# Kernel optimization log

Hardware: AMD Instinct MI355X
Metric: run time of the kernel (lower is better)

## Reference

```python
import jax, jax.numpy as jnp
import numpy as np

B, TE, TD, HE, HD = 4, 512, 256, 128, 256

def setup_inputs() -> dict:
    key = jax.random.key(0)
    k1, k2, k3, k4, k5 = jax.random.split(key, 5)
    return {
        "encoder_out_seq": jax.random.normal(k1, (B, TE, HE), dtype=jnp.float32),
        "decoder_out_seq": jax.random.normal(k2, (B, TD, HD), dtype=jnp.float32),
        "W_a": jax.random.normal(k3, (HE, HE), dtype=jnp.float32) * 0.05,
        "U_a": jax.random.normal(k4, (HD, HE), dtype=jnp.float32) * 0.05,
        "V_a": jax.random.normal(k5, (HE, 1), dtype=jnp.float32) * 0.05,
    }

def reference(encoder_out_seq, decoder_out_seq, W_a, U_a, V_a):
    # Bahdanau additive attention, fully parallel over decoder steps
    # (the original K.rnn scan has no true recurrence: each step is independent).
    Ws = jnp.einsum('bse,ef->bsf', encoder_out_seq, W_a)   # [B,Te,He]
    Uh = jnp.einsum('btd,df->btf', decoder_out_seq, U_a)   # [B,Td,He]
    # [B,Td,Te,He] additive score features
    feat = jnp.tanh(Ws[:, None, :, :] + Uh[:, :, None, :])
    e = jnp.einsum('btsf,f->bts', feat, V_a[:, 0])         # [B,Td,Te]
    e = jax.nn.softmax(e, axis=-1)                         # attention weights
    c = jnp.einsum('bts,bse->bte', e, encoder_out_seq)     # [B,Td,He] contexts
    return (c, e)
```

## Files before the change

kernel.cpp:

```cpp
#include <hip/hip_runtime.h>

#define Bn  4
#define TEn 512
#define TDn 256
#define HEn 128
#define HDn 256

#define KSCALE 2.8853900817779268f

#if __has_builtin(__builtin_amdgcn_exp2f)
#define EXP2(x) __builtin_amdgcn_exp2f(x)
#else
#define EXP2(x) __expf(0.6931471805599453f * (x))
#endif

__device__ __forceinline__ float sigEP(float E, float P) {
    return __builtin_amdgcn_rcpf(fmaf(E, P, 1.0f));
}

__global__ __launch_bounds__(512) void ws_gemm_kernel(
    const float* __restrict__ enc, const float* __restrict__ W,
    float* __restrict__ Ws)
{
    __shared__ __align__(16) float enc_lds[4 * HEn];
    const int tid = threadIdx.x;
    const int c   = tid & (HEn - 1);
    const int rl  = tid >> 7;
    const int r0  = blockIdx.x * 4;
    enc_lds[tid] = enc[r0 * HEn + tid];
    __syncthreads();
    const float* wc = W + c;
    const float* er = enc_lds + rl * HEn;
    float acc = 0.f;
    #pragma unroll 4
    for (int k = 0; k < HEn; k += 8) {
        float4 e0 = *(const float4*)(er + k);
        float4 e1 = *(const float4*)(er + k + 4);
        acc = fmaf(e0.x, wc[(k + 0) * HEn], acc);
        acc = fmaf(e0.y, wc[(k + 1) * HEn], acc);
        acc = fmaf(e0.z, wc[(k + 2) * HEn], acc);
        acc = fmaf(e0.w, wc[(k + 3) * HEn], acc);
        acc = fmaf(e1.x, wc[(k + 4) * HEn], acc);
        acc = fmaf(e1.y, wc[(k + 5) * HEn], acc);
        acc = fmaf(e1.z, wc[(k + 6) * HEn], acc);
        acc = fmaf(e1.w, wc[(k + 7) * HEn], acc);
    }
    Ws[(r0 + rl) * HEn + c] = acc * KSCALE;
}

__global__ __launch_bounds__(1024, 4) void attn_kernel(
    const float* __restrict__ enc, const float* __restrict__ dec,
    const float* __restrict__ U, const float* __restrict__ V,
    const float* __restrict__ Ws, float* __restrict__ c_out,
    float* __restrict__ e_out)
{
    const int b    = blockIdx.x >> 6;
    const int t0   = (blockIdx.x & 63) * 4;
    const int bt0  = b * TDn + t0;
    const int tid  = threadIdx.x;
    const int lane = tid & 63;
    const int wave = tid >> 6;

    __shared__ __align__(16) float dec_lds[4 * HDn];
    __shared__ __align__(16) float uh[4][HEn];
    __shared__ __align__(16) float sc[4][TEn];
    __shared__ __align__(16) float part[32][512];
    __shared__ float redm[4][8];
    __shared__ float reds[4][8];

    dec_lds[tid] = dec[bt0 * HDn + tid];
    __syncthreads();

    {
        const int f = tid & 127;
        const int p = tid >> 7;
        const float* u = U + (p * 32) * HEn + f;
        float a0 = 0.f, a1 = 0.f, a2 = 0.f, a3 = 0.f;
        #pragma unroll 8
        for (int k = 0; k < 32; ++k) {
            const float uk = u[k * HEn];
            const int kk = p * 32 + k;
            a0 = fmaf(dec_lds[kk],            uk, a0);
            a1 = fmaf(dec_lds[HDn + kk],      uk, a1);
            a2 = fmaf(dec_lds[2 * HDn + kk],  uk, a2);
            a3 = fmaf(dec_lds[3 * HDn + kk],  uk, a3);
        }
        part[p][f]       = a0;
        part[p][128 + f] = a1;
        part[p][256 + f] = a2;
        part[p][384 + f] = a3;
    }
    __syncthreads();
    if (tid < 512) {
        const int r = tid >> 7, f = tid & 127;
        float s0 = 0.f, s1 = 0.f;
        #pragma unroll
        for (int p = 0; p < 8; p += 2) {
            s0 += part[p][r * 128 + f];
            s1 += part[p + 1][r * 128 + f];
        }
        uh[r][f] = EXP2((s0 + s1) * KSCALE);
    }
    __syncthreads();

    {
        const int s_sub = lane & 7;
        const int f0    = (lane >> 3) * 16;
        float4 vn[4], uu[4][4];
        float sv = 0.f;
        #pragma unroll
        for (int j = 0; j < 4; ++j) {
            float4 v = *(const float4*)(V + f0 + 4 * j);
            sv += v.x + v.y + v.z + v.w;
            vn[j] = make_float4(-2.f * v.x, -2.f * v.y, -2.f * v.z, -2.f * v.w);
            #pragma unroll
            for (int r = 0; r < 4; ++r)
                uu[r][j] = *(const float4*)(&uh[r][f0 + 4 * j]);
        }
        const float* wsb = Ws + (b * TEn + wave * 32) * HEn;
        #pragma unroll
        for (int ci = 0; ci < 4; ++ci) {
            const float* wp = wsb + (ci * 8 + s_sub) * HEn + f0;
            float x0 = sv, x1 = sv, x2 = sv, x3 = sv;
            #pragma unroll
            for (int j = 0; j < 4; ++j) {
                float4 w = ((const float4*)wp)[j];
                const float Ex = EXP2(w.x);
                const float Ey = EXP2(w.y);
                const float Ez = EXP2(w.z);
                const float Ew = EXP2(w.w);
                x0 = fmaf(vn[j].x, sigEP(Ex, uu[0][j].x), x0);
                x1 = fmaf(vn[j].x, sigEP(Ex, uu[1][j].x), x1);
                x2 = fmaf(vn[j].x, sigEP(Ex, uu[2][j].x), x2);
                x3 = fmaf(vn[j].x, sigEP(Ex, uu[3][j].x), x3);
                x0 = fmaf(vn[j].y, sigEP(Ey, uu[0][j].y), x0);
                x1 = fmaf(vn[j].y, sigEP(Ey, uu[1][j].y), x1);
                x2 = fmaf(vn[j].y, sigEP(Ey, uu[2][j].y), x2);
                x3 = fmaf(vn[j].y, sigEP(Ey, uu[3][j].y), x3);
                x0 = fmaf(vn[j].z, sigEP(Ez, uu[0][j].z), x0);
                x1 = fmaf(vn[j].z, sigEP(Ez, uu[1][j].z), x1);
                x2 = fmaf(vn[j].z, sigEP(Ez, uu[2][j].z), x2);
                x3 = fmaf(vn[j].z, sigEP(Ez, uu[3][j].z), x3);
                x0 = fmaf(vn[j].w, sigEP(Ew, uu[0][j].w), x0);
                x1 = fmaf(vn[j].w, sigEP(Ew, uu[1][j].w), x1);
                x2 = fmaf(vn[j].w, sigEP(Ew, uu[2][j].w), x2);
                x3 = fmaf(vn[j].w, sigEP(Ew, uu[3][j].w), x3);
            }
            x0 += __shfl_xor(x0, 8, 64);  x1 += __shfl_xor(x1, 8, 64);
            x2 += __shfl_xor(x2, 8, 64);  x3 += __shfl_xor(x3, 8, 64);
            x0 += __shfl_xor(x0, 16, 64); x1 += __shfl_xor(x1, 16, 64);
            x2 += __shfl_xor(x2, 16, 64); x3 += __shfl_xor(x3, 16, 64);
            x0 += __shfl_xor(x0, 32, 64); x1 += __shfl_xor(x1, 32, 64);
            x2 += __shfl_xor(x2, 32, 64); x3 += __shfl_xor(x3, 32, 64);
            if (lane < 8) {
                const int s = wave * 32 + ci * 8 + lane;
                sc[0][s] = x0; sc[1][s] = x1; sc[2][s] = x2; sc[3][s] = x3;
            }
        }
    }
    __syncthreads();

    {
        const int s  = tid & 511;
        const int r0 = (tid >> 9) * 2;
        const int w8 = wave & 7;
        const float v0 = sc[r0][s];
        const float v1 = sc[r0 + 1][s];
        float m0 = v0, m1 = v1;
        #pragma unroll
        for (int off = 32; off; off >>= 1) {
            m0 = fmaxf(m0, __shfl_xor(m0, off, 64));
            m1 = fmaxf(m1, __shfl_xor(m1, off, 64));
        }
        if (lane == 0) { redm[r0][w8] = m0; redm[r0 + 1][w8] = m1; }
        __syncthreads();
        float bm0 = redm[r0][0], bm1 = redm[r0 + 1][0];
        #pragma unroll
        for (int w = 1; w < 8; ++w) {
            bm0 = fmaxf(bm0, redm[r0][w]);
            bm1 = fmaxf(bm1, redm[r0 + 1][w]);
        }
        const float ex0 = __expf(v0 - bm0);
        const float ex1 = __expf(v1 - bm1);
        float s0 = ex0, s1 = ex1;
        #pragma unroll
        for (int off = 32; off; off >>= 1) {
            s0 += __shfl_xor(s0, off, 64);
            s1 += __shfl_xor(s1, off, 64);
        }
        if (lane == 0) { reds[r0][w8] = s0; reds[r0 + 1][w8] = s1; }
        __syncthreads();
        float bs0 = reds[r0][0], bs1 = reds[r0 + 1][0];
        #pragma unroll
        for (int w = 1; w < 8; ++w) { bs0 += reds[r0][w]; bs1 += reds[r0 + 1][w]; }
        const float e0 = ex0 * __builtin_amdgcn_rcpf(bs0);
        const float e1 = ex1 * __builtin_amdgcn_rcpf(bs1);
        e_out[(bt0 + r0) * TEn + s]     = e0;
        e_out[(bt0 + r0 + 1) * TEn + s] = e1;
        sc[r0][s]     = e0;
        sc[r0 + 1][s] = e1;
    }
    __syncthreads();

    {
        const int hl = tid & 31;
        const int sp = tid >> 5;
        const float* eb = enc + (b * TEn + sp * 16) * HEn + hl * 4;
        float4 a0 = {0,0,0,0}, a1 = {0,0,0,0}, a2 = {0,0,0,0}, a3 = {0,0,0,0};
        #pragma unroll 4
        for (int i = 0; i < 16; ++i) {
            const int s = sp * 16 + i;
            const float4 ev = *(const float4*)(eb + i * HEn);
            const float w0 = sc[0][s], w1 = sc[1][s];
            const float w2 = sc[2][s], w3 = sc[3][s];
            a0.x = fmaf(w0, ev.x, a0.x); a1.x = fmaf(w1, ev.x, a1.x);
            a2.x = fmaf(w2, ev.x, a2.x); a3.x = fmaf(w3, ev.x, a3.x);
            a0.y = fmaf(w0, ev.y, a0.y); a1.y = fmaf(w1, ev.y, a1.y);
            a2.y = fmaf(w2, ev.y, a2.y); a3.y = fmaf(w3, ev.y, a3.y);
            a0.z = fmaf(w0, ev.z, a0.z); a1.z = fmaf(w1, ev.z, a1.z);
            a2.z = fmaf(w2, ev.z, a2.z); a3.z = fmaf(w3, ev.z, a3.z);
            a0.w = fmaf(w0, ev.w, a0.w); a1.w = fmaf(w1, ev.w, a1.w);
            a2.w = fmaf(w2, ev.w, a2.w); a3.w = fmaf(w3, ev.w, a3.w);
        }
        *(float4*)&part[sp][0   + hl * 4] = a0;
        *(float4*)&part[sp][128 + hl * 4] = a1;
        *(float4*)&part[sp][256 + hl * 4] = a2;
        *(float4*)&part[sp][384 + hl * 4] = a3;
    }
    __syncthreads();
    if (tid < 512) {
        const int r = tid >> 7, h = tid & 127;
        float s0 = 0.f, s1 = 0.f;
        #pragma unroll
        for (int p = 0; p < 32; p += 2) {
            s0 += part[p][r * 128 + h];
            s1 += part[p + 1][r * 128 + h];
        }
        c_out[(bt0 + r) * HEn + h] = s0 + s1;
    }
}

extern "C" void kernel_launch(void* const* d_in, const int* in_sizes, int n_in,
                              void* d_out, int out_size, void* d_ws, size_t ws_size,
                              hipStream_t stream) {
    const float* enc = (const float*)d_in[0];
    const float* dec = (const float*)d_in[1];
    const float* W   = (const float*)d_in[2];
    const float* U   = (const float*)d_in[3];
    const float* V   = (const float*)d_in[4];
    float* out   = (float*)d_out;
    float* c_out = out;
    float* e_out = out + Bn * TDn * HEn;
    float* Ws    = (float*)d_ws;

    ws_gemm_kernel<<<(Bn * TEn) / 4, 512, 0, stream>>>(enc, W, Ws);
    attn_kernel<<<(Bn * TDn) / 4, 1024, 0, stream>>>(enc, dec, U, V, Ws, c_out, e_out);
}
```

Baseline: 86.22 us.

## Precompute exp2 of both projections in a merged projection kernel

```diff
diff --git a/kernel.cpp b/kernel.cpp
--- a/kernel.cpp
+++ b/kernel.cpp
@@ -18,41 +18,72 @@
     return __builtin_amdgcn_rcpf(fmaf(E, P, 1.0f));
 }
 
-__global__ __launch_bounds__(512) void ws_gemm_kernel(
-    const float* __restrict__ enc, const float* __restrict__ W,
-    float* __restrict__ Ws)
+__global__ __launch_bounds__(512) void proj_kernel(
+    const float* __restrict__ enc, const float* __restrict__ dec,
+    const float* __restrict__ W, const float* __restrict__ U,
+    float* __restrict__ Ew, float* __restrict__ P)
 {
-    __shared__ __align__(16) float enc_lds[4 * HEn];
     const int tid = threadIdx.x;
-    const int c   = tid & (HEn - 1);
-    const int rl  = tid >> 7;
-    const int r0  = blockIdx.x * 4;
-    enc_lds[tid] = enc[r0 * HEn + tid];
-    __syncthreads();
-    const float* wc = W + c;
-    const float* er = enc_lds + rl * HEn;
-    float acc = 0.f;
-    #pragma unroll 4
-    for (int k = 0; k < HEn; k += 8) {
-        float4 e0 = *(const float4*)(er + k);
-        float4 e1 = *(const float4*)(er + k + 4);
-        acc = fmaf(e0.x, wc[(k + 0) * HEn], acc);
-        acc = fmaf(e0.y, wc[(k + 1) * HEn], acc);
-        acc = fmaf(e0.z, wc[(k + 2) * HEn], acc);
-        acc = fmaf(e0.w, wc[(k + 3) * HEn], acc);
-        acc = fmaf(e1.x, wc[(k + 4) * HEn], acc);
-        acc = fmaf(e1.y, wc[(k + 5) * HEn], acc);
-        acc = fmaf(e1.z, wc[(k + 6) * HEn], acc);
-        acc = fmaf(e1.w, wc[(k + 7) * HEn], acc);
-    }
-    Ws[(r0 + rl) * HEn + c] = acc * KSCALE;
+    if (blockIdx.x < 512) {
+        __shared__ __align__(16) float enc_lds[4 * HEn];
+        const int c  = tid & (HEn - 1);
+        const int rl = tid >> 7;
+        const int r0 = blockIdx.x * 4;
+        enc_lds[tid] = enc[r0 * HEn + tid];
+        __syncthreads();
+        const float* wc = W + c;
+        const float* er = enc_lds + rl * HEn;
+        float acc = 0.f;
+        #pragma unroll 4
+        for (int k = 0; k < HEn; k += 8) {
+            float4 e0 = *(const float4*)(er + k);
+            float4 e1 = *(const float4*)(er + k + 4);
+            acc = fmaf(e0.x, wc[(k + 0) * HEn], acc);
+            acc = fmaf(e0.y, wc[(k + 1) * HEn], acc);
+            acc = fmaf(e0.z, wc[(k + 2) * HEn], acc);
+            acc = fmaf(e0.w, wc[(k + 3) * HEn], acc);
+            acc = fmaf(e1.x, wc[(k + 4) * HEn], acc);
+            acc = fmaf(e1.y, wc[(k + 5) * HEn], acc);
+            acc = fmaf(e1.z, wc[(k + 6) * HEn], acc);
+            acc = fmaf(e1.w, wc[(k + 7) * HEn], acc);
+        }
+        Ew[(r0 + rl) * HEn + c] = EXP2(acc * KSCALE);
+    } else {
+        __shared__ __align__(16) float dec_lds[4 * HDn];
+        __shared__ __align__(16) float part[4][512];
+        const int bt0 = (blockIdx.x - 512) * 4;
+        dec_lds[tid]       = dec[bt0 * HDn + tid];
+        dec_lds[tid + 512] = dec[bt0 * HDn + tid + 512];
+        __syncthreads();
+        const int f = tid & 127;
+        const int p = tid >> 7;
+        const float* u = U + (p * 64) * HEn + f;
+        float a0 = 0.f, a1 = 0.f, a2 = 0.f, a3 = 0.f;
+        #pragma unroll 8
+        for (int k = 0; k < 64; ++k) {
+            const float uk = u[k * HEn];
+            const int kk = p * 64 + k;
+            a0 = fmaf(dec_lds[kk],            uk, a0);
+            a1 = fmaf(dec_lds[HDn + kk],      uk, a1);
+            a2 = fmaf(dec_lds[2 * HDn + kk],  uk, a2);
+            a3 = fmaf(dec_lds[3 * HDn + kk],  uk, a3);
+        }
+        part[p][f]       = a0;
+        part[p][128 + f] = a1;
+        part[p][256 + f] = a2;
+        part[p][384 + f] = a3;
+        __syncthreads();
+        const int r = tid >> 7;
+        const float s = part[0][r * 128 + f] + part[1][r * 128 + f]
+                      + part[2][r * 128 + f] + part[3][r * 128 + f];
+        P[(bt0 + r) * HEn + f] = EXP2(s * KSCALE);
+    }
 }
 
 __global__ __launch_bounds__(1024, 4) void attn_kernel(
-    const float* __restrict__ enc, const float* __restrict__ dec,
-    const float* __restrict__ U, const float* __restrict__ V,
-    const float* __restrict__ Ws, float* __restrict__ c_out,
-    float* __restrict__ e_out)
+    const float* __restrict__ enc, const float* __restrict__ V,
+    const float* __restrict__ Ew, const float* __restrict__ P,
+    float* __restrict__ c_out, float* __restrict__ e_out)
 {
     const int b    = blockIdx.x >> 6;
     const int t0   = (blockIdx.x & 63) * 4;
@@ -61,47 +92,10 @@
     const int lane = tid & 63;
     const int wave = tid >> 6;
 
-    __shared__ __align__(16) float dec_lds[4 * HDn];
-    __shared__ __align__(16) float uh[4][HEn];
     __shared__ __align__(16) float sc[4][TEn];
     __shared__ __align__(16) float part[32][512];
     __shared__ float redm[4][8];
     __shared__ float reds[4][8];
-
-    dec_lds[tid] = dec[bt0 * HDn + tid];
-    __syncthreads();
-
-    {
-        const int f = tid & 127;
-        const int p = tid >> 7;
-        const float* u = U + (p * 32) * HEn + f;
-        float a0 = 0.f, a1 = 0.f, a2 = 0.f, a3 = 0.f;
-        #pragma unroll 8
-        for (int k = 0; k < 32; ++k) {
-            const float uk = u[k * HEn];
-            const int kk = p * 32 + k;
-            a0 = fmaf(dec_lds[kk],            uk, a0);
-            a1 = fmaf(dec_lds[HDn + kk],      uk, a1);
-            a2 = fmaf(dec_lds[2 * HDn + kk],  uk, a2);
-            a3 = fmaf(dec_lds[3 * HDn + kk],  uk, a3);
-        }
-        part[p][f]       = a0;
-        part[p][128 + f] = a1;
-        part[p][256 + f] = a2;
-        part[p][384 + f] = a3;
-    }
-    __syncthreads();
-    if (tid < 512) {
-        const int r = tid >> 7, f = tid & 127;
-        float s0 = 0.f, s1 = 0.f;
-        #pragma unroll
-        for (int p = 0; p < 8; p += 2) {
-            s0 += part[p][r * 128 + f];
-            s1 += part[p + 1][r * 128 + f];
-        }
-        uh[r][f] = EXP2((s0 + s1) * KSCALE);
-    }
-    __syncthreads();
 
     {
         const int s_sub = lane & 7;
@@ -115,9 +109,9 @@
             vn[j] = make_float4(-2.f * v.x, -2.f * v.y, -2.f * v.z, -2.f * v.w);
             #pragma unroll
             for (int r = 0; r < 4; ++r)
-                uu[r][j] = *(const float4*)(&uh[r][f0 + 4 * j]);
-        }
-        const float* wsb = Ws + (b * TEn + wave * 32) * HEn;
+                uu[r][j] = *(const float4*)(P + (bt0 + r) * HEn + f0 + 4 * j);
+        }
+        const float* wsb = Ew + (b * TEn + wave * 32) * HEn;
         #pragma unroll
         for (int ci = 0; ci < 4; ++ci) {
             const float* wp = wsb + (ci * 8 + s_sub) * HEn + f0;
@@ -125,26 +119,22 @@
             #pragma unroll
             for (int j = 0; j < 4; ++j) {
                 float4 w = ((const float4*)wp)[j];
-                const float Ex = EXP2(w.x);
-                const float Ey = EXP2(w.y);
-                const float Ez = EXP2(w.z);
-                const float Ew = EXP2(w.w);
-                x0 = fmaf(vn[j].x, sigEP(Ex, uu[0][j].x), x0);
-                x1 = fmaf(vn[j].x, sigEP(Ex, uu[1][j].x), x1);
-                x2 = fmaf(vn[j].x, sigEP(Ex, uu[2][j].x), x2);
-                x3 = fmaf(vn[j].x, sigEP(Ex, uu[3][j].x), x3);
-                x0 = fmaf(vn[j].y, sigEP(Ey, uu[0][j].y), x0);
-                x1 = fmaf(vn[j].y, sigEP(Ey, uu[1][j].y), x1);
-                x2 = fmaf(vn[j].y, sigEP(Ey, uu[2][j].y), x2);
-                x3 = fmaf(vn[j].y, sigEP(Ey, uu[3][j].y), x3);
-                x0 = fmaf(vn[j].z, sigEP(Ez, uu[0][j].z), x0);
-                x1 = fmaf(vn[j].z, sigEP(Ez, uu[1][j].z), x1);
-                x2 = fmaf(vn[j].z, sigEP(Ez, uu[2][j].z), x2);
-                x3 = fmaf(vn[j].z, sigEP(Ez, uu[3][j].z), x3);
-                x0 = fmaf(vn[j].w, sigEP(Ew, uu[0][j].w), x0);
-                x1 = fmaf(vn[j].w, sigEP(Ew, uu[1][j].w), x1);
-                x2 = fmaf(vn[j].w, sigEP(Ew, uu[2][j].w), x2);
-                x3 = fmaf(vn[j].w, sigEP(Ew, uu[3][j].w), x3);
+                x0 = fmaf(vn[j].x, sigEP(w.x, uu[0][j].x), x0);
+                x1 = fmaf(vn[j].x, sigEP(w.x, uu[1][j].x), x1);
+                x2 = fmaf(vn[j].x, sigEP(w.x, uu[2][j].x), x2);
+                x3 = fmaf(vn[j].x, sigEP(w.x, uu[3][j].x), x3);
+                x0 = fmaf(vn[j].y, sigEP(w.y, uu[0][j].y), x0);
+                x1 = fmaf(vn[j].y, sigEP(w.y, uu[1][j].y), x1);
+                x2 = fmaf(vn[j].y, sigEP(w.y, uu[2][j].y), x2);
+                x3 = fmaf(vn[j].y, sigEP(w.y, uu[3][j].y), x3);
+                x0 = fmaf(vn[j].z, sigEP(w.z, uu[0][j].z), x0);
+                x1 = fmaf(vn[j].z, sigEP(w.z, uu[1][j].z), x1);
+                x2 = fmaf(vn[j].z, sigEP(w.z, uu[2][j].z), x2);
+                x3 = fmaf(vn[j].z, sigEP(w.z, uu[3][j].z), x3);
+                x0 = fmaf(vn[j].w, sigEP(w.w, uu[0][j].w), x0);
+                x1 = fmaf(vn[j].w, sigEP(w.w, uu[1][j].w), x1);
+                x2 = fmaf(vn[j].w, sigEP(w.w, uu[2][j].w), x2);
+                x3 = fmaf(vn[j].w, sigEP(w.w, uu[3][j].w), x3);
             }
             x0 += __shfl_xor(x0, 8, 64);  x1 += __shfl_xor(x1, 8, 64);
             x2 += __shfl_xor(x2, 8, 64);  x3 += __shfl_xor(x3, 8, 64);
@@ -251,8 +241,9 @@
     float* out   = (float*)d_out;
     float* c_out = out;
     float* e_out = out + Bn * TDn * HEn;
-    float* Ws    = (float*)d_ws;
-
-    ws_gemm_kernel<<<(Bn * TEn) / 4, 512, 0, stream>>>(enc, W, Ws);
-    attn_kernel<<<(Bn * TDn) / 4, 1024, 0, stream>>>(enc, dec, U, V, Ws, c_out, e_out);
-}
+    float* Ew    = (float*)d_ws;
+    float* P     = Ew + Bn * TEn * HEn;
+
+    proj_kernel<<<768, 512, 0, stream>>>(enc, dec, W, U, Ew, P);
+    attn_kernel<<<(Bn * TDn) / 4, 1024, 0, stream>>>(enc, V, Ew, P, c_out, e_out);
+}
```

New measurement: 86.02 us. About the same (-0.2%).
